# Optimization experiments

Hardware: AMD Instinct MI355X
Metric: run time of the kernel (lower is better)

Reference implementation:

```python
import jax, jax.numpy as jnp
import numpy as np

T1, T2 = 10.0, 50.0          # Canny hysteresis thresholds from EdgeNorm
HYST_ITERS = 16              # fixed-iteration approximation of Canny hysteresis BFS
TEMPERATURE = 1.0
NUM_CLASSES_M1 = 13.0


def _shift(a, dy, dx):
    # zero-padded shift of [n,h,w]
    p = jnp.pad(a, ((0, 0), (1, 1), (1, 1)))
    return jax.lax.dynamic_slice(p, (0, 1 + dy, 1 + dx), a.shape)


def _sobel(img):
    # img: [n,h,w] float32; replicate border, aperture-3 Sobel (cv2.Canny default)
    p = jnp.pad(img, ((0, 0), (1, 1), (1, 1)), mode='edge')[:, None]  # [n,1,h+2,w+2]
    kx = jnp.array([[-1, 0, 1], [-2, 0, 2], [-1, 0, 1]], jnp.float32)
    ky = jnp.array([[-1, -2, -1], [0, 0, 0], [1, 2, 1]], jnp.float32)
    k = jnp.stack([kx, ky])[:, None]                                  # [2,1,3,3]
    g = jax.lax.conv_general_dilated(p, k, (1, 1), 'VALID')           # [n,2,h,w]
    return g[:, 0], g[:, 1]


def _canny(img_u8):
    # vectorized Canny over the batch (cv2 loops per sample on CPU)
    img = img_u8.astype(jnp.float32)
    gx, gy = _sobel(img)
    mag = jnp.abs(gx) + jnp.abs(gy)                 # L1 magnitude (cv2 L2gradient=False)
    ang = jnp.mod(jnp.degrees(jnp.arctan2(gy, gx)), 180.0)
    s0 = (ang < 22.5) | (ang >= 157.5)
    s45 = (ang >= 22.5) & (ang < 67.5)
    s90 = (ang >= 67.5) & (ang < 112.5)
    # non-max suppression: compare along quantized gradient direction
    n1 = jnp.where(s0, _shift(mag, 0, 1),
         jnp.where(s45, _shift(mag, -1, 1),
         jnp.where(s90, _shift(mag, -1, 0), _shift(mag, -1, -1))))
    n2 = jnp.where(s0, _shift(mag, 0, -1),
         jnp.where(s45, _shift(mag, 1, -1),
         jnp.where(s90, _shift(mag, 1, 0), _shift(mag, 1, 1))))
    nms = jnp.where((mag >= n1) & (mag >= n2), mag, 0.0)
    strong = nms > T2
    weak = nms > T1

    def body(_, s):
        grown = jax.lax.reduce_window(s.astype(jnp.float32), -jnp.inf, jax.lax.max,
                                      (1, 3, 3), (1, 1, 1),
                                      [(0, 0), (1, 1), (1, 1)]) > 0.0
        return grown & weak

    strong = jax.lax.fori_loop(0, HYST_ITERS, body, strong)
    return strong.astype(jnp.float32) * 255.0       # [n,h,w] in {0,255}


def _dilate_blur(edges):
    # cv2.dilate with 10x10 ones kernel, anchor=(5,5) -> asymmetric (5,4) window pad
    d = jax.lax.reduce_window(edges, -jnp.inf, jax.lax.max,
                              (1, 10, 10), (1, 1, 1),
                              [(0, 0), (5, 4), (5, 4)])
    # cv2.blur 10x10 box filter, reflect101 border, rounded back to uint8
    p = jnp.pad(d, ((0, 0), (5, 4), (5, 4)), mode='reflect')
    b = jax.lax.reduce_window(p, 0.0, jax.lax.add,
                              (1, 10, 10), (1, 1, 1), 'VALID') / 100.0
    return jnp.round(b) / 255.0                     # EdgeNorm: e / 255


def setup_inputs() -> dict:
    key = jax.random.key(0)
    k1, k2 = jax.random.split(key)
    n, c, h, w = 8, 14, 512, 512
    return {
        'preds_S': jax.random.normal(k1, (n, c, h, w), dtype=jnp.float32),
        'preds_T': jax.random.normal(k2, (n, c, h, w), dtype=jnp.float32),
    }


def reference(preds_S, preds_T):
    n, c, h, w = preds_S.shape
    # teacher argmax map -> uint8 grayscale (truncating cast, as torch .type(uint8))
    t_map = (jnp.argmax(preds_T, axis=1).astype(jnp.float32)
             / NUM_CLASSES_M1 * 255.0).astype(jnp.uint8)
    edges = jax.lax.stop_gradient(_dilate_blur(_canny(t_map)))  # [n,h,w], constant wrt grads
    pred_T = edges[:, None] * preds_T
    pred_S = edges[:, None] * preds_S
    # ChannelNorm: softmax over flattened h*w per (n,c); divergence='kl' -> norm_s.log()
    logsm_t = jax.nn.log_softmax(pred_T.reshape(n, c, h * w), axis=-1)
    logsm_s = jax.nn.log_softmax(pred_S.reshape(n, c, h * w), axis=-1)
    norm_t = jnp.exp(logsm_t)
    loss = jnp.sum(norm_t * (logsm_t - logsm_s))    # KLDivLoss(reduction='sum')
    loss = loss / (n * c)                           # channel norm divisor
    return loss * (TEMPERATURE ** 2)
```

## Files before the change

### kernel.cpp

```cpp
#include <hip/hip_runtime.h>
#include <math.h>

#define NB 8
#define CC 14
#define HH 512
#define WW 512
#define HW (HH*WW)
#define NHW (NB*HW)
#define WPR 8
#define WPI (HH*WPR)
#define KSPLIT 32
#define KCHUNK (HW/KSPLIT)

typedef unsigned long long u64;

__global__ __launch_bounds__(256) void k_argmax(const float* __restrict__ T,
                                                uchar4* __restrict__ tmap4) {
    int i4 = blockIdx.x * blockDim.x + threadIdx.x;
    if (i4 >= NHW / 4) return;
    int n  = i4 / (HW / 4);
    int p4 = i4 - n * (HW / 4);
    const float4* base = (const float4*)(T + (size_t)n * CC * HW) + p4;
    float4 best = base[0];
    int b0 = 0, b1 = 0, b2 = 0, b3 = 0;
#pragma unroll
    for (int c = 1; c < CC; ++c) {
        float4 v = base[(size_t)c * (HW / 4)];
        if (v.x > best.x) { best.x = v.x; b0 = c; }
        if (v.y > best.y) { best.y = v.y; b1 = c; }
        if (v.z > best.z) { best.z = v.z; b2 = c; }
        if (v.w > best.w) { best.w = v.w; b3 = c; }
    }
    uchar4 g;
    g.x = (unsigned char)(((float)b0 / 13.0f) * 255.0f);
    g.y = (unsigned char)(((float)b1 / 13.0f) * 255.0f);
    g.z = (unsigned char)(((float)b2 / 13.0f) * 255.0f);
    g.w = (unsigned char)(((float)b3 / 13.0f) * 255.0f);
    tmap4[i4] = g;
}

__global__ __launch_bounds__(256) void k_sobel_nms(const unsigned char* __restrict__ tmap,
                                                   u64* __restrict__ weakBits,
                                                   u64* __restrict__ strongBits) {
    int tx = blockIdx.x, ty = blockIdx.y, n = blockIdx.z;
    int x0 = tx * 64, y0 = ty * 64;
    __shared__ unsigned char tm[68 * 68];
    __shared__ unsigned short ms[66 * 66];
    int tid = threadIdx.x;
    const unsigned char* im = tmap + (size_t)n * HW;

    for (int idx = tid; idx < 68 * 68; idx += 256) {
        int r = idx / 68, c = idx - r * 68;
        int yy = y0 - 2 + r; yy = yy < 0 ? 0 : (yy > HH - 1 ? HH - 1 : yy);
        int xx = x0 - 2 + c; xx = xx < 0 ? 0 : (xx > WW - 1 ? WW - 1 : xx);
        tm[idx] = im[yy * WW + xx];
    }
    __syncthreads();

    for (int idx = tid; idx < 66 * 66; idx += 256) {
        int r = idx / 66, c = idx - r * 66;
        const unsigned char* t0 = tm + r * 68 + c;
        int a00 = t0[0],   a01 = t0[1],   a02 = t0[2];
        int a10 = t0[68],                 a12 = t0[70];
        int a20 = t0[136], a21 = t0[137], a22 = t0[138];
        int gx = (a02 - a00) + 2 * (a12 - a10) + (a22 - a20);
        int gy = (a20 - a00) + 2 * (a21 - a01) + (a22 - a02);
        int m = (gx < 0 ? -gx : gx) + (gy < 0 ? -gy : gy);
        float ang = atan2f((float)gy, (float)gx) * 57.29577951308232f;
        ang = fmodf(ang, 180.0f);
        if (ang < 0.0f) ang += 180.0f;
        int s;
        if (ang < 22.5f || ang >= 157.5f) s = 0;
        else if (ang < 67.5f)             s = 1;
        else if (ang < 112.5f)            s = 2;
        else                              s = 3;
        ms[idx] = (unsigned short)((m << 2) | s);
    }
    __syncthreads();

    int lane = tid & 63;
    int warp = tid >> 6;
#pragma unroll
    for (int it = 0; it < 16; ++it) {
        int row = it * 4 + warp;
        int gy_ = y0 + row, gx_ = x0 + lane;
        int v = ms[(row + 1) * 66 + (lane + 1)];
        int mc = v >> 2, s = v & 3;
        int dy1, dx1, dy2, dx2;
        if (s == 0)      { dy1 = 0;  dx1 = 1;  dy2 = 0; dx2 = -1; }
        else if (s == 1) { dy1 = -1; dx1 = 1;  dy2 = 1; dx2 = -1; }
        else if (s == 2) { dy1 = -1; dx1 = 0;  dy2 = 1; dx2 = 0;  }
        else             { dy1 = -1; dx1 = -1; dy2 = 1; dx2 = 1;  }
        int y1 = gy_ + dy1, x1 = gx_ + dx1, y2 = gy_ + dy2, x2 = gx_ + dx2;
        int n1 = (y1 < 0 || y1 >= HH || x1 < 0 || x1 >= WW)
                 ? 0 : (ms[(row + 1 + dy1) * 66 + (lane + 1 + dx1)] >> 2);
        int n2 = (y2 < 0 || y2 >= HH || x2 < 0 || x2 >= WW)
                 ? 0 : (ms[(row + 1 + dy2) * 66 + (lane + 1 + dx2)] >> 2);
        int nms = (mc >= n1 && mc >= n2) ? mc : 0;
        u64 wm = __ballot(nms > 10);
        u64 sm = __ballot(nms > 50);
        if (lane == 0) {
            size_t w = (size_t)n * WPI + gy_ * WPR + tx;
            weakBits[w]   = wm;
            strongBits[w] = sm;
        }
    }
}

#define HALO 26
#define TROWS (64 + 2*HALO)
#define TWORDS (TROWS * WPR)
__global__ __launch_bounds__(1024) void k_hyst_dil_blur(const u64* __restrict__ strongBits,
                                                        const u64* __restrict__ weakBits,
                                                        float* __restrict__ E) {
    int tile = blockIdx.x & 7;
    int n    = blockIdx.x >> 3;
    int t64  = tile * 64;
    int g0   = t64 - HALO;
    __shared__ u64 A[TWORDS];
    __shared__ u64 B[TWORDS];
    __shared__ u64 Wl[TWORDS];
    __shared__ unsigned char rc[74 * 512];
    int tid = threadIdx.x;

    if (tid < TWORDS) {
        int vr = g0 + (tid >> 3);
        int w  = tid & 7;
        u64 sv = 0, wv = 0;
        if (vr >= 0 && vr < HH) {
            sv = strongBits[(size_t)n * WPI + vr * WPR + w];
            wv = weakBits  [(size_t)n * WPI + vr * WPR + w];
        }
        A[tid] = sv;
        Wl[tid] = wv;
    }
    __syncthreads();

#pragma unroll 1
    for (int it = 0; it < 16; ++it) {
        const u64* src = (it & 1) ? B : A;
        u64*       dst = (it & 1) ? A : B;
        if (tid < TWORDS) {
            int r = tid >> 3;
            int w = tid & 7;
            u64 c  = src[tid];
            u64 up = (r > 0)         ? src[tid - 8] : 0;
            u64 dn = (r < TROWS - 1) ? src[tid + 8] : 0;
            u64 a = c | up | dn;
            u64 pL = 0, pR = 0;
            if (w > 0) {
                u64 cl = src[tid - 1];
                u64 ul = (r > 0)         ? src[tid - 9] : 0;
                u64 dl = (r < TROWS - 1) ? src[tid + 7] : 0;
                pL = cl | ul | dl;
            }
            if (w < 7) {
                u64 cr = src[tid + 1];
                u64 ur = (r > 0)         ? src[tid - 7] : 0;
                u64 dr = (r < TROWS - 1) ? src[tid + 9] : 0;
                pR = cr | ur | dr;
            }
            u64 g = a | (a << 1) | (pL >> 63) | (a >> 1) | (pR << 63);
            dst[tid] = g & Wl[tid];
        }
        __syncthreads();
    }

    if (tid < TWORDS) {
        int w = tid & 7;
        u64 v  = A[tid];
        u64 p  = (w > 0) ? A[tid - 1] : 0;
        u64 nx = (w < 7) ? A[tid + 1] : 0;
        u64 o = v;
#pragma unroll
        for (int d = 1; d <= 5; ++d) o |= (v << d) | (p >> (64 - d));
#pragma unroll
        for (int d = 1; d <= 4; ++d) o |= (v >> d) | (nx << (64 - d));
        B[tid] = o;
    }
    __syncthreads();

    u64* D = Wl;
    if (tid < 74 * WPR) {
        int d = tid >> 3;
        int w = tid & 7;
        int r = d + 21;
        u64 o = 0;
#pragma unroll
        for (int dy = -5; dy <= 4; ++dy) o |= B[(r + dy) * WPR + w];
        D[d * WPR + w] = o;
    }
    __syncthreads();

    for (int idx = tid; idx < 74 * 512; idx += 1024) {
        int r = idx >> 9;
        int x = idx & 511;
        int c;
        if (x >= 5 && x <= 507) {
            int b = x - 5, wd = b >> 6, off = b & 63;
            u64 v = D[r * WPR + wd] >> off;
            if (off && wd < 7) v |= D[r * WPR + wd + 1] << (64 - off);
            c = __popcll(v & 0x3FFull);
        } else {
            c = 0;
            for (int dx = -5; dx <= 4; ++dx) {
                int xx = x + dx;
                xx = xx < 0 ? -xx : (xx > WW - 1 ? 2 * (WW - 1) - xx : xx);
                c += (int)((D[r * WPR + (xx >> 6)] >> (xx & 63)) & 1ull);
            }
        }
        rc[idx] = (unsigned char)c;
    }
    __syncthreads();

    for (int idx = tid; idx < 64 * 512; idx += 1024) {
        int yy = idx >> 9;
        int x  = idx & 511;
        int gy = t64 + yy;
        int sum = 0;
        if (gy >= 5 && gy <= HH - 5) {
#pragma unroll
            for (int k = 0; k < 10; ++k) sum += rc[(yy + k) * 512 + x];
        } else {
#pragma unroll
            for (int k = 0; k < 10; ++k) {
                int v  = gy - 5 + k;
                int rv = v < 0 ? -v : (v > HH - 1 ? 2 * (HH - 1) - v : v);
                sum += rc[(rv - (t64 - 5)) * 512 + x];
            }
        }
        float b = rintf((255.0f * (float)sum) / 100.0f);
        E[(size_t)n * HW + gy * WW + x] = b / 255.0f;
    }
}

__global__ __launch_bounds__(256) void k_kl_partial(const float* __restrict__ S,
                                                    const float* __restrict__ T,
                                                    const float* __restrict__ E,
                                                    double* __restrict__ partial) {
    int cidx  = blockIdx.x;
    int split = blockIdx.y;
    int n = cidx / CC;
    const float4* Tp = (const float4*)(T + (size_t)cidx * HW + (size_t)split * KCHUNK);
    const float4* Sp = (const float4*)(S + (size_t)cidx * HW + (size_t)split * KCHUNK);
    const float4* Ep = (const float4*)(E + (size_t)n    * HW + (size_t)split * KCHUNK);
    int tid = threadIdx.x;

    float Zt = 0.0f, Wt = 0.0f, Zs = 0.0f;
#pragma unroll
    for (int k = 0; k < KCHUNK / 4 / 256; ++k) {
        int j = k * 256 + tid;
        float4 t4 = Tp[j];
        float4 s4 = Sp[j];
        float4 e4 = Ep[j];
#pragma unroll
        for (int u = 0; u < 4; ++u) {
            float e = (&e4.x)[u];
            float t = e * (&t4.x)[u];
            float s = e * (&s4.x)[u];
            float et = __expf(t);
            Zt += et;
            Wt += et * (t - s);
            Zs += __expf(s);
        }
    }

    __shared__ double r1[256], r2[256], r3[256];
    r1[tid] = (double)Zt; r2[tid] = (double)Wt; r3[tid] = (double)Zs;
    __syncthreads();
    for (int off = 128; off > 0; off >>= 1) {
        if (tid < off) {
            r1[tid] += r1[tid + off];
            r2[tid] += r2[tid + off];
            r3[tid] += r3[tid + off];
        }
        __syncthreads();
    }
    if (tid == 0) {
        double* o = partial + ((size_t)cidx * KSPLIT + split) * 3;
        o[0] = r1[0]; o[1] = r2[0]; o[2] = r3[0];
    }
}

__global__ __launch_bounds__(128) void k_kl_final(const double* __restrict__ partial,
                                                  float* __restrict__ out) {
    int tid = threadIdx.x;
    double loss = 0.0;
    if (tid < NB * CC) {
        double Zt = 0.0, Wt = 0.0, Zs = 0.0;
        for (int sp = 0; sp < KSPLIT; ++sp) {
            const double* p = partial + ((size_t)tid * KSPLIT + sp) * 3;
            Zt += p[0]; Wt += p[1]; Zs += p[2];
        }
        loss = Wt / Zt - log(Zt) + log(Zs);
    }
    __shared__ double red[128];
    red[tid] = loss;
    __syncthreads();
    for (int off = 64; off > 0; off >>= 1) {
        if (tid < off) red[tid] += red[tid + off];
        __syncthreads();
    }
    if (tid == 0) out[0] = (float)(red[0] / (double)(NB * CC));
}

extern "C" void kernel_launch(void* const* d_in, const int* in_sizes, int n_in,
                              void* d_out, int out_size, void* d_ws, size_t ws_size,
                              hipStream_t stream) {
    const float* S = (const float*)d_in[0];
    const float* T = (const float*)d_in[1];
    float* out = (float*)d_out;

    char* ws = (char*)d_ws;
    float*         e_buf      = (float*)(ws);
    unsigned char* tmap       = (unsigned char*)(ws + (size_t)NHW * 4);
    u64*           weakBits   = (u64*)(ws + (size_t)NHW * 5);
    u64*           strongBits = (u64*)(ws + (size_t)NHW * 5 + (NHW/8));
    double*        partial    = (double*)(ws + (size_t)NHW * 5 + 2*(NHW/8));

    k_argmax<<<dim3(NHW / 4 / 256), dim3(256), 0, stream>>>(T, (uchar4*)tmap);
    k_sobel_nms<<<dim3(8, 8, NB), dim3(256), 0, stream>>>(tmap, weakBits, strongBits);
    k_hyst_dil_blur<<<dim3(NB * 8), dim3(1024), 0, stream>>>(strongBits, weakBits, e_buf);
    k_kl_partial<<<dim3(NB * CC, KSPLIT), dim3(256), 0, stream>>>(S, T, e_buf, partial);
    k_kl_final<<<1, 128, 0, stream>>>(partial, out);
    (void)in_sizes; (void)n_in; (void)out_size; (void)ws_size;
}
```

Baseline: 301.4 us.

## Store edge map as uint8, halve hysteresis tiles, fuse final KL reduction

Three changes land together. The edge weight buffer is stored as uint8 codes instead of float32, which cuts the E write and the reads in the KL pass. The hysteresis/dilate/blur kernel uses 32-row tiles, doubling the block count to 128 for better CU occupancy, at the cost of recomputing a larger relative halo. The KL block reduction now uses wavefront shuffles, and the separate final kernel is replaced by a last-block atomic counter, which removes one launch.

```diff
diff --git a/kernel.cpp b/kernel.cpp
--- a/kernel.cpp
+++ b/kernel.cpp
@@ -11,11 +11,14 @@
 #define WPI (HH*WPR)
 #define KSPLIT 32
 #define KCHUNK (HW/KSPLIT)
+#define KBLOCKS (NB*CC*KSPLIT)
 
 typedef unsigned long long u64;
 
 __global__ __launch_bounds__(256) void k_argmax(const float* __restrict__ T,
-                                                uchar4* __restrict__ tmap4) {
+                                                uchar4* __restrict__ tmap4,
+                                                unsigned* __restrict__ cnt) {
+    if (blockIdx.x == 0 && threadIdx.x == 0) *cnt = 0;
     int i4 = blockIdx.x * blockDim.x + threadIdx.x;
     if (i4 >= NHW / 4) return;
     int n  = i4 / (HW / 4);
@@ -107,20 +110,21 @@
     }
 }
 
+#define TR 32
 #define HALO 26
-#define TROWS (64 + 2*HALO)
+#define TROWS (TR + 2*HALO)
 #define TWORDS (TROWS * WPR)
 __global__ __launch_bounds__(1024) void k_hyst_dil_blur(const u64* __restrict__ strongBits,
                                                         const u64* __restrict__ weakBits,
-                                                        float* __restrict__ E) {
-    int tile = blockIdx.x & 7;
-    int n    = blockIdx.x >> 3;
-    int t64  = tile * 64;
-    int g0   = t64 - HALO;
+                                                        unsigned char* __restrict__ E) {
+    int tile = blockIdx.x & 15;
+    int n    = blockIdx.x >> 4;
+    int t0r  = tile * TR;
+    int g0   = t0r - HALO;
     __shared__ u64 A[TWORDS];
     __shared__ u64 B[TWORDS];
     __shared__ u64 Wl[TWORDS];
-    __shared__ unsigned char rc[74 * 512];
+    __shared__ unsigned char rc[(TR + 10) * 512];
     int tid = threadIdx.x;
 
     if (tid < TWORDS) {
@@ -181,10 +185,10 @@
     __syncthreads();
 
     u64* D = Wl;
-    if (tid < 74 * WPR) {
+    if (tid < (TR + 10) * WPR) {
         int d = tid >> 3;
         int w = tid & 7;
-        int r = d + 21;
+        int r = d + HALO - 5;
         u64 o = 0;
 #pragma unroll
         for (int dy = -5; dy <= 4; ++dy) o |= B[(r + dy) * WPR + w];
@@ -192,7 +196,7 @@
     }
     __syncthreads();
 
-    for (int idx = tid; idx < 74 * 512; idx += 1024) {
+    for (int idx = tid; idx < (TR + 10) * 512; idx += 1024) {
         int r = idx >> 9;
         int x = idx & 511;
         int c;
@@ -213,10 +217,10 @@
     }
     __syncthreads();
 
-    for (int idx = tid; idx < 64 * 512; idx += 1024) {
+    for (int idx = tid; idx < TR * 512; idx += 1024) {
         int yy = idx >> 9;
         int x  = idx & 511;
-        int gy = t64 + yy;
+        int gy = t0r + yy;
         int sum = 0;
         if (gy >= 5 && gy <= HH - 5) {
 #pragma unroll
@@ -226,24 +230,26 @@
             for (int k = 0; k < 10; ++k) {
                 int v  = gy - 5 + k;
                 int rv = v < 0 ? -v : (v > HH - 1 ? 2 * (HH - 1) - v : v);
-                sum += rc[(rv - (t64 - 5)) * 512 + x];
+                sum += rc[(rv - (t0r - 5)) * 512 + x];
             }
         }
         float b = rintf((255.0f * (float)sum) / 100.0f);
-        E[(size_t)n * HW + gy * WW + x] = b / 255.0f;
+        E[(size_t)n * HW + gy * WW + x] = (unsigned char)b;
     }
 }
 
 __global__ __launch_bounds__(256) void k_kl_partial(const float* __restrict__ S,
                                                     const float* __restrict__ T,
-                                                    const float* __restrict__ E,
-                                                    double* __restrict__ partial) {
+                                                    const unsigned char* __restrict__ E,
+                                                    double* __restrict__ partial,
+                                                    unsigned* __restrict__ cnt,
+                                                    float* __restrict__ out) {
     int cidx  = blockIdx.x;
     int split = blockIdx.y;
     int n = cidx / CC;
     const float4* Tp = (const float4*)(T + (size_t)cidx * HW + (size_t)split * KCHUNK);
     const float4* Sp = (const float4*)(S + (size_t)cidx * HW + (size_t)split * KCHUNK);
-    const float4* Ep = (const float4*)(E + (size_t)n    * HW + (size_t)split * KCHUNK);
+    const uchar4* Ep = (const uchar4*)(E + (size_t)n    * HW + (size_t)split * KCHUNK);
     int tid = threadIdx.x;
 
     float Zt = 0.0f, Wt = 0.0f, Zs = 0.0f;
@@ -252,10 +258,10 @@
         int j = k * 256 + tid;
         float4 t4 = Tp[j];
         float4 s4 = Sp[j];
-        float4 e4 = Ep[j];
+        uchar4 e4 = Ep[j];
 #pragma unroll
         for (int u = 0; u < 4; ++u) {
-            float e = (&e4.x)[u];
+            float e = (float)((&e4.x)[u]) / 255.0f;
             float t = e * (&t4.x)[u];
             float s = e * (&s4.x)[u];
             float et = __expf(t);
@@ -265,43 +271,51 @@
         }
     }
 
-    __shared__ double r1[256], r2[256], r3[256];
-    r1[tid] = (double)Zt; r2[tid] = (double)Wt; r3[tid] = (double)Zs;
-    __syncthreads();
-    for (int off = 128; off > 0; off >>= 1) {
-        if (tid < off) {
-            r1[tid] += r1[tid + off];
-            r2[tid] += r2[tid + off];
-            r3[tid] += r3[tid + off];
-        }
-        __syncthreads();
-    }
+    double zt = (double)Zt, wt = (double)Wt, zs = (double)Zs;
+#pragma unroll
+    for (int off = 32; off > 0; off >>= 1) {
+        zt += __shfl_down(zt, off);
+        wt += __shfl_down(wt, off);
+        zs += __shfl_down(zs, off);
+    }
+    __shared__ double wr[4][3];
+    int wv = tid >> 6, ln = tid & 63;
+    if (ln == 0) { wr[wv][0] = zt; wr[wv][1] = wt; wr[wv][2] = zs; }
+    __syncthreads();
     if (tid == 0) {
         double* o = partial + ((size_t)cidx * KSPLIT + split) * 3;
-        o[0] = r1[0]; o[1] = r2[0]; o[2] = r3[0];
-    }
-}
-
-__global__ __launch_bounds__(128) void k_kl_final(const double* __restrict__ partial,
-                                                  float* __restrict__ out) {
-    int tid = threadIdx.x;
-    double loss = 0.0;
-    if (tid < NB * CC) {
-        double Zt = 0.0, Wt = 0.0, Zs = 0.0;
-        for (int sp = 0; sp < KSPLIT; ++sp) {
-            const double* p = partial + ((size_t)tid * KSPLIT + sp) * 3;
-            Zt += p[0]; Wt += p[1]; Zs += p[2];
-        }
-        loss = Wt / Zt - log(Zt) + log(Zs);
-    }
-    __shared__ double red[128];
-    red[tid] = loss;
-    __syncthreads();
-    for (int off = 64; off > 0; off >>= 1) {
-        if (tid < off) red[tid] += red[tid + off];
+        o[0] = wr[0][0] + wr[1][0] + wr[2][0] + wr[3][0];
+        o[1] = wr[0][1] + wr[1][1] + wr[2][1] + wr[3][1];
+        o[2] = wr[0][2] + wr[1][2] + wr[2][2] + wr[3][2];
+    }
+
+    __shared__ unsigned sdone;
+    if (tid == 0) {
+        __threadfence();
+        unsigned old = atomicAdd(cnt, 1u);
+        sdone = (old == (unsigned)(KBLOCKS - 1));
+    }
+    __syncthreads();
+    if (sdone) {
+        __threadfence();
+        double loss = 0.0;
+        if (tid < NB * CC) {
+            double Ztd = 0.0, Wtd = 0.0, Zsd = 0.0;
+            for (int sp = 0; sp < KSPLIT; ++sp) {
+                const double* p = partial + ((size_t)tid * KSPLIT + sp) * 3;
+                Ztd += p[0]; Wtd += p[1]; Zsd += p[2];
+            }
+            loss = Wtd / Ztd - log(Ztd) + log(Zsd);
+        }
+        __shared__ double red[256];
+        red[tid] = loss;
         __syncthreads();
-    }
-    if (tid == 0) out[0] = (float)(red[0] / (double)(NB * CC));
+        for (int off = 128; off > 0; off >>= 1) {
+            if (tid < off) red[tid] += red[tid + off];
+            __syncthreads();
+        }
+        if (tid == 0) out[0] = (float)(red[0] / (double)(NB * CC));
+    }
 }
 
 extern "C" void kernel_launch(void* const* d_in, const int* in_sizes, int n_in,
@@ -312,16 +326,16 @@
     float* out = (float*)d_out;
 
     char* ws = (char*)d_ws;
-    float*         e_buf      = (float*)(ws);
-    unsigned char* tmap       = (unsigned char*)(ws + (size_t)NHW * 4);
-    u64*           weakBits   = (u64*)(ws + (size_t)NHW * 5);
-    u64*           strongBits = (u64*)(ws + (size_t)NHW * 5 + (NHW/8));
-    double*        partial    = (double*)(ws + (size_t)NHW * 5 + 2*(NHW/8));
-
-    k_argmax<<<dim3(NHW / 4 / 256), dim3(256), 0, stream>>>(T, (uchar4*)tmap);
+    unsigned char* e_buf      = (unsigned char*)(ws);
+    unsigned char* tmap       = (unsigned char*)(ws + (size_t)NHW);
+    u64*           weakBits   = (u64*)(ws + (size_t)NHW * 2);
+    u64*           strongBits = (u64*)(ws + (size_t)NHW * 2 + (NHW/8));
+    double*        partial    = (double*)(ws + (size_t)NHW * 2 + 2*(NHW/8));
+    unsigned*      cnt        = (unsigned*)(ws + (size_t)NHW * 2 + 2*(NHW/8) + 90112);
+
+    k_argmax<<<dim3(NHW / 4 / 256), dim3(256), 0, stream>>>(T, (uchar4*)tmap, cnt);
     k_sobel_nms<<<dim3(8, 8, NB), dim3(256), 0, stream>>>(tmap, weakBits, strongBits);
-    k_hyst_dil_blur<<<dim3(NB * 8), dim3(1024), 0, stream>>>(strongBits, weakBits, e_buf);
-    k_kl_partial<<<dim3(NB * CC, KSPLIT), dim3(256), 0, stream>>>(S, T, e_buf, partial);
-    k_kl_final<<<1, 128, 0, stream>>>(partial, out);
+    k_hyst_dil_blur<<<dim3(NB * 16), dim3(1024), 0, stream>>>(strongBits, weakBits, e_buf);
+    k_kl_partial<<<dim3(NB * CC, KSPLIT), dim3(256), 0, stream>>>(S, T, e_buf, partial, cnt, out);
     (void)in_sizes; (void)n_in; (void)out_size; (void)ws_size;
 }
```

After: 462.6 us. 53.5% more time.
